# Kernel optimization log

Measured on AMD Instinct MI355X. Metric: run time of the kernel, lower is better.

Reference implementation:

```python
import jax, jax.numpy as jnp
import numpy as np

B, N, M = 2, 2048, 8192
C1, C = 256, 128
K, SHARE = 16, 8
BN_EPS = 1e-5


def bn(x, g, b):
    # eval-mode BatchNorm1d with running_mean=0, running_var=1
    return x * (g / jnp.sqrt(1.0 + BN_EPS)) + b


def setup_inputs() -> dict:
    key = jax.random.key(0)
    ks = iter(jax.random.split(key, 64))
    nrm = lambda shape, s=0.05: jax.random.normal(next(ks), shape, dtype=jnp.float32) * s
    ones = lambda n: jnp.ones((n,), jnp.float32)
    zeros = lambda n: jnp.zeros((n,), jnp.float32)
    CS = C // SHARE  # 16
    return {
        # forward args
        "xyz": jax.random.uniform(next(ks), (B, N, 3), dtype=jnp.float32),
        "feature": jax.random.normal(next(ks), (B, C1, N), dtype=jnp.float32),
        "target_xyz": jax.random.uniform(next(ks), (B, M, 3), dtype=jnp.float32),
        "target_feature": jax.random.normal(next(ks), (B, C, M), dtype=jnp.float32),
        # TransitionUp (is_head=False): two Conv1d(k=1, bias=False)+BN+ReLU
        "tu_lin1_w": nrm((C, C1)), "tu_bn1_g": ones(C), "tu_bn1_b": zeros(C),
        "tu_lin2_w": nrm((C, C)), "tu_bn2_g": ones(C), "tu_bn2_b": zeros(C),
        # PointTransformerBlock(128,128, share_planes=8, nsample=16)
        "blk_lin1_w": nrm((C, C)), "blk_bn1_g": ones(C), "blk_bn1_b": zeros(C),
        "wq": nrm((C, C)), "bq": zeros(C),
        "wk": nrm((C, C)), "bk": zeros(C),
        "wv": nrm((C, C)), "bv": zeros(C),
        # position MLP: Linear(3,3)+BN+ReLU+Linear(3,C)
        "p1_w": nrm((3, 3), 0.3), "p1_b": zeros(3), "p_bn_g": ones(3), "p_bn_b": zeros(3),
        "p2_w": nrm((C, 3), 0.3), "p2_b": zeros(C),
        # attention weight MLP: BN(C)+ReLU+Linear(C,CS)+BN(CS)+ReLU+Linear(CS,CS)
        "w_bn1_g": ones(C), "w_bn1_b": zeros(C),
        "w_lin1_w": nrm((CS, C)), "w_lin1_b": zeros(CS),
        "w_bn2_g": ones(CS), "w_bn2_b": zeros(CS),
        "w_lin2_w": nrm((CS, CS)), "w_lin2_b": zeros(CS),
        "blk_bn2_g": ones(C), "blk_bn2_b": zeros(C),
        "blk_lin3_w": nrm((C, C)), "blk_bn3_g": ones(C), "blk_bn3_b": zeros(C),
    }


def reference(xyz, feature, target_xyz, target_feature,
              tu_lin1_w, tu_bn1_g, tu_bn1_b, tu_lin2_w, tu_bn2_g, tu_bn2_b,
              blk_lin1_w, blk_bn1_g, blk_bn1_b,
              wq, bq, wk, bk, wv, bv,
              p1_w, p1_b, p_bn_g, p_bn_b, p2_w, p2_b,
              w_bn1_g, w_bn1_b, w_lin1_w, w_lin1_b, w_bn2_g, w_bn2_b, w_lin2_w, w_lin2_b,
              blk_bn2_g, blk_bn2_b, blk_lin3_w, blk_bn3_g, blk_bn3_b):
    # ---------------- TransitionUp (feature upsampling N -> M) ----------------
    # three_nn: 3 nearest source points for each target point
    d2 = jnp.sum((target_xyz[:, :, None, :] - xyz[:, None, :, :]) ** 2, -1)  # [B,M,N]
    negd, idx3 = jax.lax.top_k(-d2, 3)                                       # [B,M,3]
    dist = jnp.sqrt(jnp.maximum(-negd, 0.0))
    rec = 1.0 / (dist + 1e-8)
    weight = rec / jnp.sum(rec, -1, keepdims=True)                           # [B,M,3]

    f = jnp.einsum('oc,bcn->bon', tu_lin1_w, feature)                        # [B,C,N]
    f = jax.nn.relu(bn(f, tu_bn1_g[None, :, None], tu_bn1_b[None, :, None]))

    # three_interpolate: weighted gather of 3-NN features
    gath = jax.vmap(lambda fb, ib: fb[:, ib])(f, idx3)                       # [B,C,M,3]
    interp = jnp.sum(gath * weight[:, None, :, :], -1)                       # [B,C,M]

    tf = jnp.einsum('oc,bcm->bom', tu_lin2_w, target_feature)
    tf = jax.nn.relu(bn(tf, tu_bn2_g[None, :, None], tu_bn2_b[None, :, None]))
    feat = tf + interp                                                        # [B,C,M]

    # ---------------- PointTransformerBlock (local kNN vector attention) ----------------
    x = feat.transpose(0, 2, 1)                                               # [B,M,C]
    identity = x
    x1 = jax.nn.relu(bn(x @ blk_lin1_w.T, blk_bn1_g, blk_bn1_b))              # [B,M,C]

    # kNN among target points (includes self, distance 0)
    d2t = jnp.sum((target_xyz[:, :, None, :] - target_xyz[:, None, :, :]) ** 2, -1)  # [B,M,M]
    _, knn = jax.lax.top_k(-d2t, K)                                           # [B,M,K]

    q = x1 @ wq.T + bq
    k = x1 @ wk.T + bk
    v = x1 @ wv.T + bv
    gather_nb = jax.vmap(lambda tb, ib: tb[ib])                               # [M,C],[M,K] -> [M,K,C]
    xk = gather_nb(k, knn)                                                    # [B,M,K,C]
    xv = gather_nb(v, knn)                                                    # [B,M,K,C]

    # relative positional encoding
    pr = gather_nb(target_xyz, knn) - target_xyz[:, :, None, :]               # [B,M,K,3]
    pr = jax.nn.relu(bn(pr @ p1_w.T + p1_b, p_bn_g, p_bn_b)) @ p2_w.T + p2_b  # [B,M,K,C]

    r = xk - q[:, :, None, :] + pr                                            # [B,M,K,C]
    w = jax.nn.relu(bn(r, w_bn1_g, w_bn1_b)) @ w_lin1_w.T + w_lin1_b          # [B,M,K,CS]
    w = jax.nn.relu(bn(w, w_bn2_g, w_bn2_b)) @ w_lin2_w.T + w_lin2_b          # [B,M,K,CS]
    w = jax.nn.softmax(w, axis=2)                                             # over K neighbors

    CS = C // SHARE
    agg = jnp.sum((xv + pr).reshape(B, M, K, SHARE, CS) * w[:, :, :, None, :], axis=2)
    agg = agg.reshape(B, M, C)

    x2 = jax.nn.relu(bn(agg, blk_bn2_g, blk_bn2_b))
    x3 = bn(x2 @ blk_lin3_w.T, blk_bn3_g, blk_bn3_b)
    out = jax.nn.relu(x3 + identity)                                          # [B,M,C]
    return out.transpose(0, 2, 1)                                             # [B,C,M]
```

## Files before the change

### kernel.cpp

```cpp
#include <hip/hip_runtime.h>
#include <cstddef>
#include <cstdint>

#define B_  2
#define N_  2048
#define M_  8192
#define C1_ 256
#define C_  128
#define K_  16
#define CS_ 16

#define BNINV 0.9999950000374997f

#define LDSA 17
#define LDSB 33

__device__ __forceinline__ void stage_direct64(float4* Ls4, const float4* src4,
                                               size_t row_stride4, int k0,
                                               size_t col0_4, int t)
{
#pragma unroll
    for (int i = 0; i < 2; ++i) {
        int idx = t + i * 256;
        int kk = idx >> 4, f4 = idx & 15;
        Ls4[kk * LDSA + f4] = src4[(size_t)(k0 + kk) * row_stride4 + col0_4 + f4];
    }
}

__device__ __forceinline__ void stage_transposeA(float* Lsf, const float* src,
                                                 int row0, int ldk, int k0, int t)
{
    int u = t & 7, r = t >> 3;
#pragma unroll
    for (int i = 0; i < 2; ++i) {
        int row = r + i * 32;
        float4 v = *(const float4*)(src + (size_t)(row0 + row) * ldk + k0 + u * 4);
        Lsf[(u * 4 + 0) * 68 + row] = v.x;
        Lsf[(u * 4 + 1) * 68 + row] = v.y;
        Lsf[(u * 4 + 2) * 68 + row] = v.z;
        Lsf[(u * 4 + 3) * 68 + row] = v.w;
    }
}

__device__ __forceinline__ void stage_transposeB(float* Lsf, const float* src,
                                                 int ldk, int k0, int t)
{
    int u = t & 7, r = t >> 3;
#pragma unroll
    for (int i = 0; i < 4; ++i) {
        int row = r + i * 32;
        float4 v = *(const float4*)(src + (size_t)row * ldk + k0 + u * 4);
        Lsf[(u * 4 + 0) * 132 + row] = v.x;
        Lsf[(u * 4 + 1) * 132 + row] = v.y;
        Lsf[(u * 4 + 2) * 132 + row] = v.z;
        Lsf[(u * 4 + 3) * 132 + row] = v.w;
    }
}

__device__ __forceinline__ void gemm_step64(const float4* As4, const float4* Bs4,
                                            int tm, int tn, float acc[4][8])
{
#pragma unroll 4
    for (int kk = 0; kk < 32; ++kk) {
        float4 a0 = As4[kk * LDSA + tm];
        float4 b0 = Bs4[kk * LDSB + tn * 2];
        float4 b1 = Bs4[kk * LDSB + tn * 2 + 1];
        float av[4] = {a0.x,a0.y,a0.z,a0.w};
        float bv[8] = {b0.x,b0.y,b0.z,b0.w,b1.x,b1.y,b1.z,b1.w};
#pragma unroll
        for (int i = 0; i < 4; ++i)
#pragma unroll
            for (int j = 0; j < 8; ++j)
                acc[i][j] = fmaf(av[i], bv[j], acc[i][j]);
    }
}

__device__ __forceinline__ void load8(const float* p, float* v)
{
    float4 a = *(const float4*)p, b = *(const float4*)(p + 4);
    v[0]=a.x; v[1]=a.y; v[2]=a.z; v[3]=a.w; v[4]=b.x; v[5]=b.y; v[6]=b.z; v[7]=b.w;
}
__device__ __forceinline__ void store8(float* p, const float* v)
{
    *(float4*)p       = make_float4(v[0],v[1],v[2],v[3]);
    *(float4*)(p + 4) = make_float4(v[4],v[5],v[6],v[7]);
}

extern "C" __global__ __launch_bounds__(256) void k_f(
    const float* __restrict__ feature, const float* __restrict__ w,
    const float* __restrict__ g, const float* __restrict__ bb,
    float* __restrict__ f_t)
{
    __shared__ float4 As4[32 * LDSA], Bs4[32 * LDSB];
    int t = threadIdx.x, tm = t >> 4, tn = t & 15;
    int m0 = blockIdx.x * 64;
    int b = m0 >> 11;
    size_t col0_4 = (size_t)(m0 & (N_ - 1)) >> 2;
    const float4* src4 = (const float4*)feature + (size_t)b * C1_ * (N_ / 4);
    float acc[4][8] = {};
    for (int k0 = 0; k0 < C1_; k0 += 32) {
        stage_direct64(As4, src4, N_ / 4, k0, col0_4, t);
        stage_transposeB((float*)Bs4, w, C1_, k0, t);
        __syncthreads();
        gemm_step64(As4, Bs4, tm, tn, acc);
        __syncthreads();
    }
    int c0 = tn * 8;
    float gc[8], bc[8];
    load8(g + c0, gc); load8(bb + c0, bc);
#pragma unroll
    for (int mm = 0; mm < 4; ++mm) {
        int m = m0 + tm * 4 + mm;
        float o[8];
#pragma unroll
        for (int j = 0; j < 8; ++j)
            o[j] = fmaxf(fmaf(acc[mm][j], gc[j] * BNINV, bc[j]), 0.f);
        store8(f_t + (size_t)m * C_ + c0, o);
    }
}

extern "C" __global__ __launch_bounds__(256) void k_soa(
    const float* __restrict__ txyz,
    float* __restrict__ cx, float* __restrict__ cy, float* __restrict__ cz)
{
    int t = blockIdx.x * 256 + threadIdx.x;
    if (t < B_ * M_) {
        cx[t] = txyz[t*3+0];
        cy[t] = txyz[t*3+1];
        cz[t] = txyz[t*3+2];
    }
}

extern "C" __global__ __launch_bounds__(256) void k_three_nn(
    const float* __restrict__ xyz, const float* __restrict__ txyz,
    int* __restrict__ idx3, float* __restrict__ w3)
{
    int q    = blockIdx.x * 4 + (threadIdx.x >> 6);
    int lane = threadIdx.x & 63;
    int b    = q / M_;
    const float* src = xyz + (size_t)b * N_ * 3;
    float qx = txyz[(size_t)q*3+0], qy = txyz[(size_t)q*3+1], qz = txyz[(size_t)q*3+2];

    unsigned long long p0 = ~0ULL, p1 = ~0ULL, p2 = ~0ULL;
    for (int i = 0; i < N_/64; ++i) {
        int j = lane + (i << 6);
        float dx = src[j*3+0]-qx, dy = src[j*3+1]-qy, dz = src[j*3+2]-qz;
        float d = __fadd_rn(__fadd_rn(__fmul_rn(dx,dx), __fmul_rn(dy,dy)), __fmul_rn(dz,dz));
        unsigned long long key = ((unsigned long long)__float_as_uint(d) << 32) | (unsigned)j;
        if (key < p2) {
            p2 = key;
            if (p2 < p1) { unsigned long long t = p1; p1 = p2; p2 = t; }
            if (p1 < p0) { unsigned long long t = p0; p0 = p1; p1 = t; }
        }
    }
    unsigned long long wmin[3];
    unsigned long long h = p0;
#pragma unroll
    for (int r = 0; r < 3; ++r) {
        unsigned long long w = h;
#pragma unroll
        for (int s = 1; s < 64; s <<= 1) {
            unsigned long long o = __shfl_xor(w, s, 64);
            w = (o < w) ? o : w;
        }
        wmin[r] = w;
        if (h == w) { p0 = p1; p1 = p2; p2 = ~0ULL; h = p0; }
    }
    if (lane == 0) {
        float d0 = __uint_as_float((unsigned)(wmin[0] >> 32));
        float d1 = __uint_as_float((unsigned)(wmin[1] >> 32));
        float d2 = __uint_as_float((unsigned)(wmin[2] >> 32));
        float s0 = sqrtf(fmaxf(d0, 0.f)), s1 = sqrtf(fmaxf(d1, 0.f)), s2 = sqrtf(fmaxf(d2, 0.f));
        float r0 = 1.f/(s0+1e-8f), r1 = 1.f/(s1+1e-8f), r2 = 1.f/(s2+1e-8f);
        float inv = 1.f/(r0+r1+r2);
        idx3[(size_t)q*3+0] = (int)(unsigned)wmin[0];
        idx3[(size_t)q*3+1] = (int)(unsigned)wmin[1];
        idx3[(size_t)q*3+2] = (int)(unsigned)wmin[2];
        w3[(size_t)q*3+0] = r0*inv; w3[(size_t)q*3+1] = r1*inv; w3[(size_t)q*3+2] = r2*inv;
    }
}

extern "C" __global__ __launch_bounds__(256) void k_feat(
    const float* __restrict__ tfeat, const float* __restrict__ w2,
    const float* __restrict__ g, const float* __restrict__ bb,
    const float* __restrict__ f_t, const int* __restrict__ idx3,
    const float* __restrict__ w3, float* __restrict__ x)
{
    __shared__ float4 As4[32 * LDSA], Bs4[32 * LDSB];
    int t = threadIdx.x, tm = t >> 4, tn = t & 15;
    int m0 = blockIdx.x * 64;
    int b = m0 >> 13;
    size_t col0_4 = (size_t)(m0 & (M_ - 1)) >> 2;
    const float4* src4 = (const float4*)tfeat + (size_t)b * C_ * (M_ / 4);
    float acc[4][8] = {};
    for (int k0 = 0; k0 < C_; k0 += 32) {
        stage_direct64(As4, src4, M_ / 4, k0, col0_4, t);
        stage_transposeB((float*)Bs4, w2, C_, k0, t);
        __syncthreads();
        gemm_step64(As4, Bs4, tm, tn, acc);
        __syncthreads();
    }
    int c0 = tn * 8;
    float gc[8], bc[8];
    load8(g + c0, gc); load8(bb + c0, bc);
    const float* fb = f_t + (size_t)b * N_ * C_;
#pragma unroll
    for (int mm = 0; mm < 4; ++mm) {
        int m = m0 + tm * 4 + mm;
        int   i0 = idx3[m*3+0], i1 = idx3[m*3+1], i2 = idx3[m*3+2];
        float u0 = w3[m*3+0],  u1 = w3[m*3+1],  u2 = w3[m*3+2];
        float r0[8], r1[8], r2[8];
        load8(fb + (size_t)i0 * C_ + c0, r0);
        load8(fb + (size_t)i1 * C_ + c0, r1);
        load8(fb + (size_t)i2 * C_ + c0, r2);
        float o[8];
#pragma unroll
        for (int j = 0; j < 8; ++j) {
            float y = fmaxf(fmaf(acc[mm][j], gc[j] * BNINV, bc[j]), 0.f);
            o[j] = y + u0 * r0[j] + u1 * r1[j] + u2 * r2[j];
        }
        store8(x + (size_t)m * C_ + c0, o);
    }
}

extern "C" __global__ __launch_bounds__(256) void k_knn(
    const float* __restrict__ cx, const float* __restrict__ cy,
    const float* __restrict__ cz, int* __restrict__ out_knn)
{
    int q    = blockIdx.x * 4 + (threadIdx.x >> 6);
    int lane = threadIdx.x & 63;
    int b    = q >> 13;
    const float4* bx4 = (const float4*)(cx + (size_t)b * M_);
    const float4* by4 = (const float4*)(cy + (size_t)b * M_);
    const float4* bz4 = (const float4*)(cz + (size_t)b * M_);
    float qx = cx[q], qy = cy[q], qz = cz[q];

    unsigned long long list = ~0ULL;
    unsigned long long tau  = ~0ULL;
    float taud = 3e38f;

#define DIST(px,py,pz) ({ \
    float dx = (px)-qx, dy = (py)-qy, dz = (pz)-qz; \
    __fadd_rn(__fadd_rn(__fmul_rn(dx,dx), __fmul_rn(dy,dy)), __fmul_rn(dz,dz)); })

#define MIN4 (min(min(k0,k1),min(k2,k3)))

#define MERGELOOP { \
    unsigned long long mask = __ballot(mk < tau); \
    while (mask) { \
        int srcl = (int)__ffsll((long long)mask) - 1; \
        unsigned long long kk = __shfl(mk, srcl, 64); \
        unsigned long long below = __ballot(list < kk) & 0xFFFFull; \
        int pos = __popcll(below); \
        unsigned long long sh = __shfl_up(list, 1, 64); \
        if (lane == pos)                  list = kk; \
        else if (lane > pos && lane < K_) list = sh; \
        tau = __shfl(list, K_ - 1, 64); \
        if (lane == srcl) { \
            if      (k0 == mk) k0 = ~0ULL; \
            else if (k1 == mk) k1 = ~0ULL; \
            else if (k2 == mk) k2 = ~0ULL; \
            else               k3 = ~0ULL; \
            mk = MIN4; \
        } \
        mask = __ballot(mk < tau); \
    } \
    taud = __uint_as_float((unsigned)(tau >> 32)); }

    {
        float4 px = bx4[lane], py = by4[lane], pz = bz4[lane];
        float d0 = DIST(px.x,py.x,pz.x);
        float d1 = DIST(px.y,py.y,pz.y);
        float d2 = DIST(px.z,py.z,pz.z);
        float d3 = DIST(px.w,py.w,pz.w);
        unsigned long long j0 = (unsigned)(lane*4);
        unsigned long long k0 = ((unsigned long long)__float_as_uint(d0) << 32) | (j0+0);
        unsigned long long k1 = ((unsigned long long)__float_as_uint(d1) << 32) | (j0+1);
        unsigned long long k2 = ((unsigned long long)__float_as_uint(d2) << 32) | (j0+2);
        unsigned long long k3 = ((unsigned long long)__float_as_uint(d3) << 32) | (j0+3);
        unsigned long long key = k0;
#pragma unroll
        for (int k = 2; k <= 64; k <<= 1) {
#pragma unroll
            for (int j = k >> 1; j > 0; j >>= 1) {
                unsigned long long o = __shfl_xor(key, j, 64);
                bool up  = ((lane & k) == 0);
                bool low = ((lane & j) == 0);
                bool keepmin = (low == up);
                unsigned long long mn = (o < key) ? o : key;
                unsigned long long mx = (o < key) ? key : o;
                key = keepmin ? mn : mx;
            }
        }
        if (lane < K_) list = key;
        tau  = __shfl(list, K_ - 1, 64);
        taud = __uint_as_float((unsigned)(tau >> 32));
        k0 = ~0ULL;
        unsigned long long mk = MIN4;
        MERGELOOP
    }

    for (int i = 1; i < M_/256; ++i) {
        float4 px = bx4[i*64 + lane];
        float4 py = by4[i*64 + lane];
        float4 pz = bz4[i*64 + lane];
        float d0 = DIST(px.x,py.x,pz.x);
        float d1 = DIST(px.y,py.y,pz.y);
        float d2 = DIST(px.z,py.z,pz.z);
        float d3 = DIST(px.w,py.w,pz.w);
        bool any = (d0 <= taud) | (d1 <= taud) | (d2 <= taud) | (d3 <= taud);
        if (__ballot(any)) {
            unsigned long long j0 = (unsigned)(i*256 + lane*4);
            unsigned long long k0 = ((unsigned long long)__float_as_uint(d0) << 32) | (j0+0);
            unsigned long long k1 = ((unsigned long long)__float_as_uint(d1) << 32) | (j0+1);
            unsigned long long k2 = ((unsigned long long)__float_as_uint(d2) << 32) | (j0+2);
            unsigned long long k3 = ((unsigned long long)__float_as_uint(d3) << 32) | (j0+3);
            unsigned long long mk = MIN4;
            MERGELOOP
        }
    }
#undef MERGELOOP
#undef MIN4
#undef DIST
    if (lane < K_)
        out_knn[(size_t)q*K_ + lane] = (int)(unsigned)list;
}

extern "C" __global__ __launch_bounds__(256) void k_lqkv(
    const float* __restrict__ xin,
    const float* __restrict__ w1, const float* __restrict__ g1, const float* __restrict__ b1,
    const float* __restrict__ wq, const float* __restrict__ bq,
    const float* __restrict__ wk, const float* __restrict__ bk,
    const float* __restrict__ wv, const float* __restrict__ bv,
    float* __restrict__ q, float* __restrict__ k, float* __restrict__ v)
{
    __shared__ float  Asf[128 * 68];
    __shared__ float4 Bs4[32 * LDSB];
    int t = threadIdx.x, tm = t >> 4, tn = t & 15;
    int m0 = blockIdx.x * 64;
    int c0 = tn * 8;

    for (int k0 = 0; k0 < C_; k0 += 32)
        stage_transposeA(Asf + k0 * 68, xin, m0, C_, k0, t);

    float acc[4][8] = {};
    for (int k0 = 0; k0 < C_; k0 += 32) {
        stage_transposeB((float*)Bs4, w1, C_, k0, t);
        __syncthreads();
        gemm_step64((const float4*)Asf + k0 * 17, Bs4, tm, tn, acc);
        __syncthreads();
    }
    {
        float gc[8], bc[8];
        load8(g1 + c0, gc); load8(b1 + c0, bc);
#pragma unroll
        for (int mm = 0; mm < 4; ++mm) {
            int ml = tm * 4 + mm;
#pragma unroll
            for (int j = 0; j < 8; ++j)
                Asf[(c0 + j) * 68 + ml] = fmaxf(fmaf(acc[mm][j], gc[j] * BNINV, bc[j]), 0.f);
        }
    }
    __syncthreads();

#pragma unroll 1
    for (int which = 0; which < 3; ++which) {
        const float* W  = (which == 0) ? wq : (which == 1) ? wk : wv;
        const float* bi = (which == 0) ? bq : (which == 1) ? bk : bv;
        float*       out= (which == 0) ? q  : (which == 1) ? k  : v;
        float acc2[4][8] = {};
        for (int k0 = 0; k0 < C_; k0 += 32) {
            stage_transposeB((float*)Bs4, W, C_, k0, t);
            __syncthreads();
            gemm_step64((const float4*)Asf + k0 * 17, Bs4, tm, tn, acc2);
            __syncthreads();
        }
        float bc[8];
        load8(bi + c0, bc);
#pragma unroll
        for (int mm = 0; mm < 4; ++mm) {
            int m = m0 + tm * 4 + mm;
            float o[8];
#pragma unroll
            for (int j = 0; j < 8; ++j) o[j] = acc2[mm][j] + bc[j];
            store8(out + (size_t)m * C_ + c0, o);
        }
    }
}

extern "C" __global__ __launch_bounds__(128) void k_attn2(
    const float* __restrict__ q, const float* __restrict__ kf, const float* __restrict__ vf,
    const int* __restrict__ knn, const float* __restrict__ txyz,
    const float* __restrict__ p1w, const float* __restrict__ p1b,
    const float* __restrict__ pbg, const float* __restrict__ pbb,
    const float* __restrict__ p2w, const float* __restrict__ p2b,
    const float* __restrict__ wb1g, const float* __restrict__ wb1b,
    const float* __restrict__ wl1, const float* __restrict__ wl1b,
    const float* __restrict__ wb2g, const float* __restrict__ wb2b,
    const float* __restrict__ wl2, const float* __restrict__ wl2b,
    const float* __restrict__ bn2g, const float* __restrict__ bn2b,
    float* __restrict__ x2out)
{
    __shared__ int   nbs[K_];
    __shared__ float scrd[K_][3];
    __shared__ float tshs[K_ * C_];
    __shared__ float svs [K_ * C_];
    __shared__ float wl1s[CS_ * 132];
    __shared__ float wl2s[CS_ * 17];
    __shared__ float ashs[K_ * 17];
    __shared__ float wshs[K_ * 17];

    int bm = blockIdx.x;
    int b  = bm >> 13;
    int c  = threadIdx.x;

#pragma unroll
    for (int i = 0; i < 16; ++i) {
        int idx = c + i * 128;
        wl1s[(idx >> 7) * 132 + (idx & 127)] = wl1[idx];
    }
    {
        int i1 = c, i2 = c + 128;
        if (i1 < 256) wl2s[(i1 >> 4) * 17 + (i1 & 15)] = wl2[i1];
        if (i2 < 256) wl2s[(i2 >> 4) * 17 + (i2 & 15)] = wl2[i2];
    }
    if (c < K_) nbs[c] = knn[(size_t)bm * K_ + c];
    __syncthreads();

    float kfv[K_], vfv[K_];
    const float* txb = txyz + (size_t)b * M_ * 3;
#pragma unroll
    for (int t = 0; t < K_; ++t) {
        size_t nrow = ((size_t)b * M_ + nbs[t]) * C_ + c;
        kfv[t] = kf[nrow];
        vfv[t] = vf[nrow];
    }
    if (c < 48) {
        int t = c / 3, comp = c - t * 3;
        scrd[t][comp] = txb[nbs[t] * 3 + comp];
    }

    float qc = q[(size_t)bm * C_ + c];
    float qx = txyz[(size_t)bm*3+0], qy = txyz[(size_t)bm*3+1], qz = txyz[(size_t)bm*3+2];
    float p2w0 = p2w[c*3+0], p2w1 = p2w[c*3+1], p2w2 = p2w[c*3+2], p2bc = p2b[c];
    float b1s = wb1g[c]*BNINV, b1b = wb1b[c];
    float a00=p1w[0],a01=p1w[1],a02=p1w[2],a10=p1w[3],a11=p1w[4],a12=p1w[5],a20=p1w[6],a21=p1w[7],a22=p1w[8];
    float pb0=p1b[0], pb1=p1b[1], pb2=p1b[2];
    float g0=pbg[0]*BNINV, g1=pbg[1]*BNINV, g2=pbg[2]*BNINV;
    float hb0=pbb[0], hb1=pbb[1], hb2=pbb[2];
    __syncthreads();

#pragma unroll
    for (int t = 0; t < K_; ++t) {
        float dx = scrd[t][0]-qx, dy = scrd[t][1]-qy, dz = scrd[t][2]-qz;
        float h0 = fmaxf(fmaf(fmaf(a02,dz, fmaf(a01,dy, fmaf(a00,dx, pb0))), g0, hb0), 0.f);
        float h1 = fmaxf(fmaf(fmaf(a12,dz, fmaf(a11,dy, fmaf(a10,dx, pb1))), g1, hb1), 0.f);
        float h2 = fmaxf(fmaf(fmaf(a22,dz, fmaf(a21,dy, fmaf(a20,dx, pb2))), g2, hb2), 0.f);
        float pr = fmaf(p2w2,h2, fmaf(p2w1,h1, fmaf(p2w0,h0, p2bc)));
        float r = kfv[t] - qc + pr;
        tshs[t*C_ + c] = fmaxf(fmaf(r, b1s, b1b), 0.f);
        svs [t*C_ + c] = vfv[t] + pr;
    }
    __syncthreads();

    {
        int s = c >> 3, u = c & 7;
        float w1b = wl1b[s], gg = wb2g[s]*BNINV, gb = wb2b[s];
        for (int nb = 0; nb < K_; ++nb) {
            float a = 0.f;
#pragma unroll
            for (int i = 0; i < 16; ++i)
                a = fmaf(wl1s[s*132 + u + 8*i], tshs[nb*C_ + u + 8*i], a);
            a += __shfl_down(a, 4, 8);
            a += __shfl_down(a, 2, 8);
            a += __shfl_down(a, 1, 8);
            if (u == 0)
                ashs[nb*17 + s] = fmaxf(fmaf(a + w1b, gg, gb), 0.f);
        }
    }
    __syncthreads();

    {
        int nb = c >> 3;
        int cs1 = c & 7, cs2 = (c & 7) + 8;
        float a1 = wl2b[cs1], a2 = wl2b[cs2];
#pragma unroll
        for (int j = 0; j < CS_; ++j) {
            float av = ashs[nb*17 + j];
            a1 = fmaf(wl2s[cs1*17 + j], av, a1);
            a2 = fmaf(wl2s[cs2*17 + j], av, a2);
        }
        wshs[nb*17 + cs1] = a1;
        wshs[nb*17 + cs2] = a2;
    }
    __syncthreads();

    if (c < CS_) {
        float mx = -3e38f;
#pragma unroll
        for (int nb = 0; nb < K_; ++nb) mx = fmaxf(mx, wshs[nb*17 + c]);
        float ssum = 0.f;
#pragma unroll
        for (int nb = 0; nb < K_; ++nb) {
            float e = __expf(wshs[nb*17 + c] - mx);
            wshs[nb*17 + c] = e; ssum += e;
        }
        float inv = 1.f / ssum;
#pragma unroll
        for (int nb = 0; nb < K_; ++nb) wshs[nb*17 + c] *= inv;
    }
    __syncthreads();

    float agg = 0.f;
    int cs = c & (CS_ - 1);
#pragma unroll
    for (int nb = 0; nb < K_; ++nb)
        agg = fmaf(svs[nb*C_ + c], wshs[nb*17 + cs], agg);
    float x2 = fmaxf(fmaf(agg, bn2g[c]*BNINV, bn2b[c]), 0.f);
    x2out[(size_t)bm * C_ + c] = x2;
}

extern "C" __global__ __launch_bounds__(256) void k_lin3(
    const float* __restrict__ x2, const float* __restrict__ w,
    const float* __restrict__ g, const float* __restrict__ bb,
    const float* __restrict__ xid, float* __restrict__ out)
{
    __shared__ float4 As4[32 * LDSA], Bs4[32 * LDSB];
    int t = threadIdx.x, tm = t >> 4, tn = t & 15;
    int m0 = blockIdx.x * 64;
    int b  = m0 >> 13;
    float acc[4][8] = {};
    for (int k0 = 0; k0 < C_; k0 += 32) {
        stage_transposeA((float*)As4, x2, m0, C_, k0, t);
        stage_transposeB((float*)Bs4, w, C_, k0, t);
        __syncthreads();
        gemm_step64(As4, Bs4, tm, tn, acc);
        __syncthreads();
    }
    int c0 = tn * 8;
    float gc[8], bc[8];
    load8(g + c0, gc); load8(bb + c0, bc);
#pragma unroll
    for (int mm = 0; mm < 4; ++mm) {
        int m = m0 + tm * 4 + mm;
        float idv[8];
        load8(xid + (size_t)m * C_ + c0, idv);
#pragma unroll
        for (int j = 0; j < 8; ++j) {
            float x3 = fmaf(acc[mm][j], gc[j] * BNINV, bc[j]);
            acc[mm][j] = fmaxf(x3 + idv[j], 0.f);
        }
    }
    int mloc = (m0 & (M_ - 1)) + tm * 4;
    float* ob = out + (size_t)b * C_ * M_;
#pragma unroll
    for (int j = 0; j < 8; ++j) {
        float* p = ob + (size_t)(c0 + j) * M_ + mloc;
        *(float4*)p = make_float4(acc[0][j], acc[1][j], acc[2][j], acc[3][j]);
    }
}

extern "C" void kernel_launch(void* const* d_in, const int* in_sizes, int n_in,
                              void* d_out, int out_size, void* d_ws, size_t ws_size,
                              hipStream_t stream)
{
    const float* xyz   = (const float*)d_in[0];
    const float* feat  = (const float*)d_in[1];
    const float* txyz  = (const float*)d_in[2];
    const float* tfeat = (const float*)d_in[3];
    const float* tu1w  = (const float*)d_in[4];
    const float* tu1g  = (const float*)d_in[5];
    const float* tu1b  = (const float*)d_in[6];
    const float* tu2w  = (const float*)d_in[7];
    const float* tu2g  = (const float*)d_in[8];
    const float* tu2b  = (const float*)d_in[9];
    const float* bl1w  = (const float*)d_in[10];
    const float* bl1g  = (const float*)d_in[11];
    const float* bl1b  = (const float*)d_in[12];
    const float* wq    = (const float*)d_in[13];
    const float* bq    = (const float*)d_in[14];
    const float* wk    = (const float*)d_in[15];
    const float* bk    = (const float*)d_in[16];
    const float* wv    = (const float*)d_in[17];
    const float* bv    = (const float*)d_in[18];
    const float* p1w   = (const float*)d_in[19];
    const float* p1b   = (const float*)d_in[20];
    const float* pbg   = (const float*)d_in[21];
    const float* pbb   = (const float*)d_in[22];
    const float* p2w   = (const float*)d_in[23];
    const float* p2b   = (const float*)d_in[24];
    const float* wb1g  = (const float*)d_in[25];
    const float* wb1b  = (const float*)d_in[26];
    const float* wl1   = (const float*)d_in[27];
    const float* wl1b  = (const float*)d_in[28];
    const float* wb2g  = (const float*)d_in[29];
    const float* wb2b  = (const float*)d_in[30];
    const float* wl2   = (const float*)d_in[31];
    const float* wl2b  = (const float*)d_in[32];
    const float* bn2g  = (const float*)d_in[33];
    const float* bn2b  = (const float*)d_in[34];
    const float* l3w   = (const float*)d_in[35];
    const float* bn3g  = (const float*)d_in[36];
    const float* bn3b  = (const float*)d_in[37];

    char* ws = (char*)d_ws;
    size_t off = 0;
    auto alloc = [&](size_t bytes) { void* p = ws + off; off += (bytes + 255) & ~(size_t)255; return p; };
    float* f_t  = (float*)alloc(sizeof(float) * B_ * N_ * C_);
    int*   idx3 = (int*)  alloc(sizeof(int)   * B_ * M_ * 3);
    float* w3   = (float*)alloc(sizeof(float) * B_ * M_ * 3);
    float* x    = (float*)alloc(sizeof(float) * B_ * M_ * C_);
    float* x2   = (float*)alloc(sizeof(float) * B_ * M_ * C_);
    float* qb   = (float*)alloc(sizeof(float) * B_ * M_ * C_);
    float* kb   = (float*)alloc(sizeof(float) * B_ * M_ * C_);
    float* vb   = (float*)alloc(sizeof(float) * B_ * M_ * C_);
    int*   knn  = (int*)  alloc(sizeof(int)   * B_ * M_ * K_);
    float* cx   = (float*)alloc(sizeof(float) * B_ * M_);
    float* cy   = (float*)alloc(sizeof(float) * B_ * M_);
    float* cz   = (float*)alloc(sizeof(float) * B_ * M_);

    k_soa     <<<(B_*M_+255)/256, 256, 0, stream>>>(txyz, cx, cy, cz);
    k_f       <<<B_*N_/64,        256, 0, stream>>>(feat, tu1w, tu1g, tu1b, f_t);
    k_three_nn<<<B_*M_/4,         256, 0, stream>>>(xyz, txyz, idx3, w3);
    k_feat    <<<B_*M_/64,        256, 0, stream>>>(tfeat, tu2w, tu2g, tu2b, f_t, idx3, w3, x);
    k_knn     <<<B_*M_/4,         256, 0, stream>>>(cx, cy, cz, knn);
    k_lqkv    <<<B_*M_/64,        256, 0, stream>>>(x, bl1w, bl1g, bl1b,
                                                    wq, bq, wk, bk, wv, bv, qb, kb, vb);
    k_attn2   <<<B_*M_,           128, 0, stream>>>(qb, kb, vb, knn, txyz,
                                                    p1w, p1b, pbg, pbb, p2w, p2b,
                                                    wb1g, wb1b, wl1, wl1b, wb2g, wb2b, wl2, wl2b,
                                                    bn2g, bn2b, x2);
    k_lin3    <<<B_*M_/64,        256, 0, stream>>>(x2, l3w, bn3g, bn3b, x, (float*)d_out);
}
```

Measured before the change: 374.0 us.

## Fuse independent kernels into heterogeneous launches splitting kNN across stages

The self-kNN search is split into three block ranges and co-scheduled inside three combined kernels, alongside the feature GEMM plus three-NN, the interpolation GEMM, and the QKV projection. Block index selects which body runs, so independent work fills the GPU concurrently instead of running serially. This removes launch gaps and tail underutilisation. The cost is a uniform register and LDS footprint across both roles, which may reduce occupancy for the lighter kNN blocks.

```diff
diff --git a/kernel.cpp b/kernel.cpp
--- a/kernel.cpp
+++ b/kernel.cpp
@@ -12,6 +12,14 @@
 
 #define BNINV 0.9999950000374997f
 
+#define KNN1 1024
+#define KNN2 2048
+#define KNN3 1024
+#define FB    (B_*N_/64)
+#define TNNB  (B_*M_/4)
+#define FEATB (B_*M_/64)
+#define LQKVB (B_*M_/64)
+
 #define LDSA 17
 #define LDSB 33
 
@@ -86,149 +94,13 @@
     *(float4*)(p + 4) = make_float4(v[4],v[5],v[6],v[7]);
 }
 
-extern "C" __global__ __launch_bounds__(256) void k_f(
-    const float* __restrict__ feature, const float* __restrict__ w,
-    const float* __restrict__ g, const float* __restrict__ bb,
-    float* __restrict__ f_t)
-{
-    __shared__ float4 As4[32 * LDSA], Bs4[32 * LDSB];
-    int t = threadIdx.x, tm = t >> 4, tn = t & 15;
-    int m0 = blockIdx.x * 64;
-    int b = m0 >> 11;
-    size_t col0_4 = (size_t)(m0 & (N_ - 1)) >> 2;
-    const float4* src4 = (const float4*)feature + (size_t)b * C1_ * (N_ / 4);
-    float acc[4][8] = {};
-    for (int k0 = 0; k0 < C1_; k0 += 32) {
-        stage_direct64(As4, src4, N_ / 4, k0, col0_4, t);
-        stage_transposeB((float*)Bs4, w, C1_, k0, t);
-        __syncthreads();
-        gemm_step64(As4, Bs4, tm, tn, acc);
-        __syncthreads();
-    }
-    int c0 = tn * 8;
-    float gc[8], bc[8];
-    load8(g + c0, gc); load8(bb + c0, bc);
-#pragma unroll
-    for (int mm = 0; mm < 4; ++mm) {
-        int m = m0 + tm * 4 + mm;
-        float o[8];
-#pragma unroll
-        for (int j = 0; j < 8; ++j)
-            o[j] = fmaxf(fmaf(acc[mm][j], gc[j] * BNINV, bc[j]), 0.f);
-        store8(f_t + (size_t)m * C_ + c0, o);
-    }
-}
-
-extern "C" __global__ __launch_bounds__(256) void k_soa(
-    const float* __restrict__ txyz,
-    float* __restrict__ cx, float* __restrict__ cy, float* __restrict__ cz)
-{
-    int t = blockIdx.x * 256 + threadIdx.x;
-    if (t < B_ * M_) {
-        cx[t] = txyz[t*3+0];
-        cy[t] = txyz[t*3+1];
-        cz[t] = txyz[t*3+2];
-    }
-}
-
-extern "C" __global__ __launch_bounds__(256) void k_three_nn(
-    const float* __restrict__ xyz, const float* __restrict__ txyz,
-    int* __restrict__ idx3, float* __restrict__ w3)
-{
-    int q    = blockIdx.x * 4 + (threadIdx.x >> 6);
-    int lane = threadIdx.x & 63;
-    int b    = q / M_;
-    const float* src = xyz + (size_t)b * N_ * 3;
-    float qx = txyz[(size_t)q*3+0], qy = txyz[(size_t)q*3+1], qz = txyz[(size_t)q*3+2];
-
-    unsigned long long p0 = ~0ULL, p1 = ~0ULL, p2 = ~0ULL;
-    for (int i = 0; i < N_/64; ++i) {
-        int j = lane + (i << 6);
-        float dx = src[j*3+0]-qx, dy = src[j*3+1]-qy, dz = src[j*3+2]-qz;
-        float d = __fadd_rn(__fadd_rn(__fmul_rn(dx,dx), __fmul_rn(dy,dy)), __fmul_rn(dz,dz));
-        unsigned long long key = ((unsigned long long)__float_as_uint(d) << 32) | (unsigned)j;
-        if (key < p2) {
-            p2 = key;
-            if (p2 < p1) { unsigned long long t = p1; p1 = p2; p2 = t; }
-            if (p1 < p0) { unsigned long long t = p0; p0 = p1; p1 = t; }
-        }
-    }
-    unsigned long long wmin[3];
-    unsigned long long h = p0;
-#pragma unroll
-    for (int r = 0; r < 3; ++r) {
-        unsigned long long w = h;
-#pragma unroll
-        for (int s = 1; s < 64; s <<= 1) {
-            unsigned long long o = __shfl_xor(w, s, 64);
-            w = (o < w) ? o : w;
-        }
-        wmin[r] = w;
-        if (h == w) { p0 = p1; p1 = p2; p2 = ~0ULL; h = p0; }
-    }
-    if (lane == 0) {
-        float d0 = __uint_as_float((unsigned)(wmin[0] >> 32));
-        float d1 = __uint_as_float((unsigned)(wmin[1] >> 32));
-        float d2 = __uint_as_float((unsigned)(wmin[2] >> 32));
-        float s0 = sqrtf(fmaxf(d0, 0.f)), s1 = sqrtf(fmaxf(d1, 0.f)), s2 = sqrtf(fmaxf(d2, 0.f));
-        float r0 = 1.f/(s0+1e-8f), r1 = 1.f/(s1+1e-8f), r2 = 1.f/(s2+1e-8f);
-        float inv = 1.f/(r0+r1+r2);
-        idx3[(size_t)q*3+0] = (int)(unsigned)wmin[0];
-        idx3[(size_t)q*3+1] = (int)(unsigned)wmin[1];
-        idx3[(size_t)q*3+2] = (int)(unsigned)wmin[2];
-        w3[(size_t)q*3+0] = r0*inv; w3[(size_t)q*3+1] = r1*inv; w3[(size_t)q*3+2] = r2*inv;
-    }
-}
-
-extern "C" __global__ __launch_bounds__(256) void k_feat(
-    const float* __restrict__ tfeat, const float* __restrict__ w2,
-    const float* __restrict__ g, const float* __restrict__ bb,
-    const float* __restrict__ f_t, const int* __restrict__ idx3,
-    const float* __restrict__ w3, float* __restrict__ x)
-{
-    __shared__ float4 As4[32 * LDSA], Bs4[32 * LDSB];
-    int t = threadIdx.x, tm = t >> 4, tn = t & 15;
-    int m0 = blockIdx.x * 64;
-    int b = m0 >> 13;
-    size_t col0_4 = (size_t)(m0 & (M_ - 1)) >> 2;
-    const float4* src4 = (const float4*)tfeat + (size_t)b * C_ * (M_ / 4);
-    float acc[4][8] = {};
-    for (int k0 = 0; k0 < C_; k0 += 32) {
-        stage_direct64(As4, src4, M_ / 4, k0, col0_4, t);
-        stage_transposeB((float*)Bs4, w2, C_, k0, t);
-        __syncthreads();
-        gemm_step64(As4, Bs4, tm, tn, acc);
-        __syncthreads();
-    }
-    int c0 = tn * 8;
-    float gc[8], bc[8];
-    load8(g + c0, gc); load8(bb + c0, bc);
-    const float* fb = f_t + (size_t)b * N_ * C_;
-#pragma unroll
-    for (int mm = 0; mm < 4; ++mm) {
-        int m = m0 + tm * 4 + mm;
-        int   i0 = idx3[m*3+0], i1 = idx3[m*3+1], i2 = idx3[m*3+2];
-        float u0 = w3[m*3+0],  u1 = w3[m*3+1],  u2 = w3[m*3+2];
-        float r0[8], r1[8], r2[8];
-        load8(fb + (size_t)i0 * C_ + c0, r0);
-        load8(fb + (size_t)i1 * C_ + c0, r1);
-        load8(fb + (size_t)i2 * C_ + c0, r2);
-        float o[8];
-#pragma unroll
-        for (int j = 0; j < 8; ++j) {
-            float y = fmaxf(fmaf(acc[mm][j], gc[j] * BNINV, bc[j]), 0.f);
-            o[j] = y + u0 * r0[j] + u1 * r1[j] + u2 * r2[j];
-        }
-        store8(x + (size_t)m * C_ + c0, o);
-    }
-}
-
-extern "C" __global__ __launch_bounds__(256) void k_knn(
-    const float* __restrict__ cx, const float* __restrict__ cy,
-    const float* __restrict__ cz, int* __restrict__ out_knn)
-{
-    int q    = blockIdx.x * 4 + (threadIdx.x >> 6);
-    int lane = threadIdx.x & 63;
+
+__device__ void knn_body(const float* __restrict__ cx, const float* __restrict__ cy,
+                         const float* __restrict__ cz, int* __restrict__ out_knn,
+                         int qblock, int tid)
+{
+    int q    = qblock * 4 + (tid >> 6);
+    int lane = tid & 63;
     int b    = q >> 13;
     const float4* bx4 = (const float4*)(cx + (size_t)b * M_);
     const float4* by4 = (const float4*)(cy + (size_t)b * M_);
@@ -326,18 +198,140 @@
         out_knn[(size_t)q*K_ + lane] = (int)(unsigned)list;
 }
 
-extern "C" __global__ __launch_bounds__(256) void k_lqkv(
-    const float* __restrict__ xin,
-    const float* __restrict__ w1, const float* __restrict__ g1, const float* __restrict__ b1,
-    const float* __restrict__ wq, const float* __restrict__ bq,
-    const float* __restrict__ wk, const float* __restrict__ bk,
-    const float* __restrict__ wv, const float* __restrict__ bv,
-    float* __restrict__ q, float* __restrict__ k, float* __restrict__ v)
-{
-    __shared__ float  Asf[128 * 68];
-    __shared__ float4 Bs4[32 * LDSB];
-    int t = threadIdx.x, tm = t >> 4, tn = t & 15;
-    int m0 = blockIdx.x * 64;
+__device__ void f_body(const float* __restrict__ feature, const float* __restrict__ w,
+                       const float* __restrict__ g, const float* __restrict__ bb,
+                       float* __restrict__ f_t, int m0, int t, char* smem)
+{
+    float4* As4 = (float4*)smem;
+    float4* Bs4 = (float4*)(smem + 32 * LDSA * 16);
+    int tm = t >> 4, tn = t & 15;
+    int b = m0 >> 11;
+    size_t col0_4 = (size_t)(m0 & (N_ - 1)) >> 2;
+    const float4* src4 = (const float4*)feature + (size_t)b * C1_ * (N_ / 4);
+    float acc[4][8] = {};
+    for (int k0 = 0; k0 < C1_; k0 += 32) {
+        stage_direct64(As4, src4, N_ / 4, k0, col0_4, t);
+        stage_transposeB((float*)Bs4, w, C1_, k0, t);
+        __syncthreads();
+        gemm_step64(As4, Bs4, tm, tn, acc);
+        __syncthreads();
+    }
+    int c0 = tn * 8;
+    float gc[8], bc[8];
+    load8(g + c0, gc); load8(bb + c0, bc);
+#pragma unroll
+    for (int mm = 0; mm < 4; ++mm) {
+        int m = m0 + tm * 4 + mm;
+        float o[8];
+#pragma unroll
+        for (int j = 0; j < 8; ++j)
+            o[j] = fmaxf(fmaf(acc[mm][j], gc[j] * BNINV, bc[j]), 0.f);
+        store8(f_t + (size_t)m * C_ + c0, o);
+    }
+}
+
+__device__ void tnn_body(const float* __restrict__ xyz, const float* __restrict__ txyz,
+                         int* __restrict__ idx3, float* __restrict__ w3,
+                         int q, int lane)
+{
+    int b = q / M_;
+    const float* src = xyz + (size_t)b * N_ * 3;
+    float qx = txyz[(size_t)q*3+0], qy = txyz[(size_t)q*3+1], qz = txyz[(size_t)q*3+2];
+
+    unsigned long long p0 = ~0ULL, p1 = ~0ULL, p2 = ~0ULL;
+    for (int i = 0; i < N_/64; ++i) {
+        int j = lane + (i << 6);
+        float dx = src[j*3+0]-qx, dy = src[j*3+1]-qy, dz = src[j*3+2]-qz;
+        float d = __fadd_rn(__fadd_rn(__fmul_rn(dx,dx), __fmul_rn(dy,dy)), __fmul_rn(dz,dz));
+        unsigned long long key = ((unsigned long long)__float_as_uint(d) << 32) | (unsigned)j;
+        if (key < p2) {
+            p2 = key;
+            if (p2 < p1) { unsigned long long t = p1; p1 = p2; p2 = t; }
+            if (p1 < p0) { unsigned long long t = p0; p0 = p1; p1 = t; }
+        }
+    }
+    unsigned long long wmin[3];
+    unsigned long long h = p0;
+#pragma unroll
+    for (int r = 0; r < 3; ++r) {
+        unsigned long long w = h;
+#pragma unroll
+        for (int s = 1; s < 64; s <<= 1) {
+            unsigned long long o = __shfl_xor(w, s, 64);
+            w = (o < w) ? o : w;
+        }
+        wmin[r] = w;
+        if (h == w) { p0 = p1; p1 = p2; p2 = ~0ULL; h = p0; }
+    }
+    if (lane == 0) {
+        float d0 = __uint_as_float((unsigned)(wmin[0] >> 32));
+        float d1 = __uint_as_float((unsigned)(wmin[1] >> 32));
+        float d2 = __uint_as_float((unsigned)(wmin[2] >> 32));
+        float s0 = sqrtf(fmaxf(d0, 0.f)), s1 = sqrtf(fmaxf(d1, 0.f)), s2 = sqrtf(fmaxf(d2, 0.f));
+        float r0 = 1.f/(s0+1e-8f), r1 = 1.f/(s1+1e-8f), r2 = 1.f/(s2+1e-8f);
+        float inv = 1.f/(r0+r1+r2);
+        idx3[(size_t)q*3+0] = (int)(unsigned)wmin[0];
+        idx3[(size_t)q*3+1] = (int)(unsigned)wmin[1];
+        idx3[(size_t)q*3+2] = (int)(unsigned)wmin[2];
+        w3[(size_t)q*3+0] = r0*inv; w3[(size_t)q*3+1] = r1*inv; w3[(size_t)q*3+2] = r2*inv;
+    }
+}
+
+__device__ void feat_body(const float* __restrict__ tfeat, const float* __restrict__ w2,
+                          const float* __restrict__ g, const float* __restrict__ bb,
+                          const float* __restrict__ f_t, const int* __restrict__ idx3,
+                          const float* __restrict__ w3, float* __restrict__ x,
+                          int m0, int t, char* smem)
+{
+    float4* As4 = (float4*)smem;
+    float4* Bs4 = (float4*)(smem + 32 * LDSA * 16);
+    int tm = t >> 4, tn = t & 15;
+    int b = m0 >> 13;
+    size_t col0_4 = (size_t)(m0 & (M_ - 1)) >> 2;
+    const float4* src4 = (const float4*)tfeat + (size_t)b * C_ * (M_ / 4);
+    float acc[4][8] = {};
+    for (int k0 = 0; k0 < C_; k0 += 32) {
+        stage_direct64(As4, src4, M_ / 4, k0, col0_4, t);
+        stage_transposeB((float*)Bs4, w2, C_, k0, t);
+        __syncthreads();
+        gemm_step64(As4, Bs4, tm, tn, acc);
+        __syncthreads();
+    }
+    int c0 = tn * 8;
+    float gc[8], bc[8];
+    load8(g + c0, gc); load8(bb + c0, bc);
+    const float* fb = f_t + (size_t)b * N_ * C_;
+#pragma unroll
+    for (int mm = 0; mm < 4; ++mm) {
+        int m = m0 + tm * 4 + mm;
+        int   i0 = idx3[m*3+0], i1 = idx3[m*3+1], i2 = idx3[m*3+2];
+        float u0 = w3[m*3+0],  u1 = w3[m*3+1],  u2 = w3[m*3+2];
+        float r0[8], r1[8], r2[8];
+        load8(fb + (size_t)i0 * C_ + c0, r0);
+        load8(fb + (size_t)i1 * C_ + c0, r1);
+        load8(fb + (size_t)i2 * C_ + c0, r2);
+        float o[8];
+#pragma unroll
+        for (int j = 0; j < 8; ++j) {
+            float y = fmaxf(fmaf(acc[mm][j], gc[j] * BNINV, bc[j]), 0.f);
+            o[j] = y + u0 * r0[j] + u1 * r1[j] + u2 * r2[j];
+        }
+        store8(x + (size_t)m * C_ + c0, o);
+    }
+}
+
+__device__ void lqkv_body(const float* __restrict__ xin,
+                          const float* __restrict__ w1, const float* __restrict__ g1,
+                          const float* __restrict__ b1,
+                          const float* __restrict__ wq, const float* __restrict__ bq,
+                          const float* __restrict__ wk, const float* __restrict__ bk,
+                          const float* __restrict__ wv, const float* __restrict__ bv,
+                          float* __restrict__ q, float* __restrict__ k, float* __restrict__ v,
+                          int m0, int t, char* smem)
+{
+    float*  Asf = (float*)smem;
+    float4* Bs4 = (float4*)(smem + 128 * 68 * 4);
+    int tm = t >> 4, tn = t & 15;
     int c0 = tn * 8;
 
     for (int k0 = 0; k0 < C_; k0 += 32)
@@ -386,6 +380,73 @@
             store8(out + (size_t)m * C_ + c0, o);
         }
     }
+}
+
+
+extern "C" __global__ __launch_bounds__(256) void k_soa(
+    const float* __restrict__ txyz,
+    float* __restrict__ cx, float* __restrict__ cy, float* __restrict__ cz)
+{
+    int t = blockIdx.x * 256 + threadIdx.x;
+    if (t < B_ * M_) {
+        cx[t] = txyz[t*3+0];
+        cy[t] = txyz[t*3+1];
+        cz[t] = txyz[t*3+2];
+    }
+}
+
+extern "C" __global__ __launch_bounds__(256) void k_fat1(
+    const float* __restrict__ cx, const float* __restrict__ cy,
+    const float* __restrict__ cz, int* __restrict__ out_knn,
+    const float* __restrict__ feature, const float* __restrict__ w,
+    const float* __restrict__ g, const float* __restrict__ bb,
+    float* __restrict__ f_t,
+    const float* __restrict__ xyz, const float* __restrict__ txyz,
+    int* __restrict__ idx3, float* __restrict__ w3)
+{
+    __shared__ __align__(16) char smem[32 * LDSA * 16 + 32 * LDSB * 16];
+    int bid = blockIdx.x, tid = threadIdx.x;
+    if (bid < KNN1)
+        knn_body(cx, cy, cz, out_knn, bid, tid);
+    else if (bid < KNN1 + FB)
+        f_body(feature, w, g, bb, f_t, (bid - KNN1) * 64, tid, smem);
+    else
+        tnn_body(xyz, txyz, idx3, w3, (bid - KNN1 - FB) * 4 + (tid >> 6), tid & 63);
+}
+
+extern "C" __global__ __launch_bounds__(256) void k_fat2(
+    const float* __restrict__ cx, const float* __restrict__ cy,
+    const float* __restrict__ cz, int* __restrict__ out_knn,
+    const float* __restrict__ tfeat, const float* __restrict__ w2,
+    const float* __restrict__ g, const float* __restrict__ bb,
+    const float* __restrict__ f_t, const int* __restrict__ idx3,
+    const float* __restrict__ w3, float* __restrict__ x)
+{
+    __shared__ __align__(16) char smem[32 * LDSA * 16 + 32 * LDSB * 16];
+    int bid = blockIdx.x, tid = threadIdx.x;
+    if (bid < KNN2)
+        knn_body(cx, cy, cz, out_knn, KNN1 + bid, tid);
+    else
+        feat_body(tfeat, w2, g, bb, f_t, idx3, w3, x, (bid - KNN2) * 64, tid, smem);
+}
+
+extern "C" __global__ __launch_bounds__(256) void k_fat3(
+    const float* __restrict__ cx, const float* __restrict__ cy,
+    const float* __restrict__ cz, int* __restrict__ out_knn,
+    const float* __restrict__ xin,
+    const float* __restrict__ w1, const float* __restrict__ g1, const float* __restrict__ b1,
+    const float* __restrict__ wq, const float* __restrict__ bq,
+    const float* __restrict__ wk, const float* __restrict__ bk,
+    const float* __restrict__ wv, const float* __restrict__ bv,
+    float* __restrict__ q, float* __restrict__ k, float* __restrict__ v)
+{
+    __shared__ __align__(16) char smem[128 * 68 * 4 + 32 * LDSB * 16];
+    int bid = blockIdx.x, tid = threadIdx.x;
+    if (bid < KNN3)
+        knn_body(cx, cy, cz, out_knn, KNN1 + KNN2 + bid, tid);
+    else
+        lqkv_body(xin, w1, g1, b1, wq, bq, wk, bk, wv, bv, q, k, v,
+                  (bid - KNN3) * 64, tid, smem);
 }
 
 extern "C" __global__ __launch_bounds__(128) void k_attn2(
@@ -619,16 +680,19 @@
     float* cy   = (float*)alloc(sizeof(float) * B_ * M_);
     float* cz   = (float*)alloc(sizeof(float) * B_ * M_);
 
-    k_soa     <<<(B_*M_+255)/256, 256, 0, stream>>>(txyz, cx, cy, cz);
-    k_f       <<<B_*N_/64,        256, 0, stream>>>(feat, tu1w, tu1g, tu1b, f_t);
-    k_three_nn<<<B_*M_/4,         256, 0, stream>>>(xyz, txyz, idx3, w3);
-    k_feat    <<<B_*M_/64,        256, 0, stream>>>(tfeat, tu2w, tu2g, tu2b, f_t, idx3, w3, x);
-    k_knn     <<<B_*M_/4,         256, 0, stream>>>(cx, cy, cz, knn);
-    k_lqkv    <<<B_*M_/64,        256, 0, stream>>>(x, bl1w, bl1g, bl1b,
-                                                    wq, bq, wk, bk, wv, bv, qb, kb, vb);
-    k_attn2   <<<B_*M_,           128, 0, stream>>>(qb, kb, vb, knn, txyz,
-                                                    p1w, p1b, pbg, pbb, p2w, p2b,
-                                                    wb1g, wb1b, wl1, wl1b, wb2g, wb2b, wl2, wl2b,
-                                                    bn2g, bn2b, x2);
-    k_lin3    <<<B_*M_/64,        256, 0, stream>>>(x2, l3w, bn3g, bn3b, x, (float*)d_out);
-}
+    k_soa  <<<(B_*M_+255)/256,     256, 0, stream>>>(txyz, cx, cy, cz);
+    k_fat1 <<<KNN1 + FB + TNNB,    256, 0, stream>>>(cx, cy, cz, knn,
+                                                     feat, tu1w, tu1g, tu1b, f_t,
+                                                     xyz, txyz, idx3, w3);
+    k_fat2 <<<KNN2 + FEATB,        256, 0, stream>>>(cx, cy, cz, knn,
+                                                     tfeat, tu2w, tu2g, tu2b,
+                                                     f_t, idx3, w3, x);
+    k_fat3 <<<KNN3 + LQKVB,        256, 0, stream>>>(cx, cy, cz, knn,
+                                                     x, bl1w, bl1g, bl1b,
+                                                     wq, bq, wk, bk, wv, bv, qb, kb, vb);
+    k_attn2<<<B_*M_,               128, 0, stream>>>(qb, kb, vb, knn, txyz,
+                                                     p1w, p1b, pbg, pbb, p2w, p2b,
+                                                     wb1g, wb1b, wl1, wl1b, wb2g, wb2b, wl2, wl2b,
+                                                     bn2g, bn2b, x2);
+    k_lin3 <<<B_*M_/64,            256, 0, stream>>>(x2, l3w, bn3g, bn3b, x, (float*)d_out);
+}
```

Result: slower. 427.7 us (+14.4%).

## Process two query points per attention block and keep value rows in registers

Applied to the files above, without the earlier changes.

The attention kernel now handles two target points per 256-thread block instead of one per 128-thread block. This halves the number of times the shared wl1/wl2 weight tiles are loaded into LDS per point. The value-plus-positional term is also kept in registers instead of a shared svs array, which removes that LDS traffic and its footprint. In exchange the per-block LDS for tshs/ashs/wshs doubles and register pressure rises slightly, which may change occupancy.

```diff
diff --git a/kernel.cpp b/kernel.cpp
--- a/kernel.cpp
+++ b/kernel.cpp
@@ -388,7 +388,7 @@
     }
 }
 
-extern "C" __global__ __launch_bounds__(128) void k_attn2(
+extern "C" __global__ __launch_bounds__(256) void k_attn2(
     const float* __restrict__ q, const float* __restrict__ kf, const float* __restrict__ vf,
     const int* __restrict__ knn, const float* __restrict__ txyz,
     const float* __restrict__ p1w, const float* __restrict__ p1b,
@@ -401,43 +401,40 @@
     const float* __restrict__ bn2g, const float* __restrict__ bn2b,
     float* __restrict__ x2out)
 {
-    __shared__ int   nbs[K_];
-    __shared__ float scrd[K_][3];
-    __shared__ float tshs[K_ * C_];
-    __shared__ float svs [K_ * C_];
+    __shared__ int   nbs[2][K_];
+    __shared__ float scrd[2][K_][3];
+    __shared__ float tshs[2][K_ * C_];
     __shared__ float wl1s[CS_ * 132];
     __shared__ float wl2s[CS_ * 17];
-    __shared__ float ashs[K_ * 17];
-    __shared__ float wshs[K_ * 17];
-
-    int bm = blockIdx.x;
-    int b  = bm >> 13;
-    int c  = threadIdx.x;
-
-#pragma unroll
-    for (int i = 0; i < 16; ++i) {
-        int idx = c + i * 128;
+    __shared__ float ashs[2][K_ * 17];
+    __shared__ float wshs[2][K_ * 17];
+
+    int tid = threadIdx.x;
+    int p   = tid >> 7;
+    int c   = tid & 127;
+    int bm  = blockIdx.x * 2 + p;
+    int b   = bm >> 13;
+
+#pragma unroll
+    for (int i = 0; i < 8; ++i) {
+        int idx = tid + i * 256;
         wl1s[(idx >> 7) * 132 + (idx & 127)] = wl1[idx];
     }
-    {
-        int i1 = c, i2 = c + 128;
-        if (i1 < 256) wl2s[(i1 >> 4) * 17 + (i1 & 15)] = wl2[i1];
-        if (i2 < 256) wl2s[(i2 >> 4) * 17 + (i2 & 15)] = wl2[i2];
-    }
-    if (c < K_) nbs[c] = knn[(size_t)bm * K_ + c];
+    wl2s[(tid >> 4) * 17 + (tid & 15)] = wl2[tid & 255];
+    if (c < K_) nbs[p][c] = knn[(size_t)bm * K_ + c];
     __syncthreads();
 
-    float kfv[K_], vfv[K_];
+    float kfv[K_], svr[K_];
     const float* txb = txyz + (size_t)b * M_ * 3;
 #pragma unroll
     for (int t = 0; t < K_; ++t) {
-        size_t nrow = ((size_t)b * M_ + nbs[t]) * C_ + c;
+        size_t nrow = ((size_t)b * M_ + nbs[p][t]) * C_ + c;
         kfv[t] = kf[nrow];
-        vfv[t] = vf[nrow];
+        svr[t] = vf[nrow];
     }
     if (c < 48) {
         int t = c / 3, comp = c - t * 3;
-        scrd[t][comp] = txb[nbs[t] * 3 + comp];
+        scrd[p][t][comp] = txb[nbs[p][t] * 3 + comp];
     }
 
     float qc = q[(size_t)bm * C_ + c];
@@ -452,14 +449,14 @@
 
 #pragma unroll
     for (int t = 0; t < K_; ++t) {
-        float dx = scrd[t][0]-qx, dy = scrd[t][1]-qy, dz = scrd[t][2]-qz;
+        float dx = scrd[p][t][0]-qx, dy = scrd[p][t][1]-qy, dz = scrd[p][t][2]-qz;
         float h0 = fmaxf(fmaf(fmaf(a02,dz, fmaf(a01,dy, fmaf(a00,dx, pb0))), g0, hb0), 0.f);
         float h1 = fmaxf(fmaf(fmaf(a12,dz, fmaf(a11,dy, fmaf(a10,dx, pb1))), g1, hb1), 0.f);
         float h2 = fmaxf(fmaf(fmaf(a22,dz, fmaf(a21,dy, fmaf(a20,dx, pb2))), g2, hb2), 0.f);
         float pr = fmaf(p2w2,h2, fmaf(p2w1,h1, fmaf(p2w0,h0, p2bc)));
         float r = kfv[t] - qc + pr;
-        tshs[t*C_ + c] = fmaxf(fmaf(r, b1s, b1b), 0.f);
-        svs [t*C_ + c] = vfv[t] + pr;
+        tshs[p][t*C_ + c] = fmaxf(fmaf(r, b1s, b1b), 0.f);
+        svr[t] += pr;
     }
     __syncthreads();
 
@@ -470,12 +467,12 @@
             float a = 0.f;
 #pragma unroll
             for (int i = 0; i < 16; ++i)
-                a = fmaf(wl1s[s*132 + u + 8*i], tshs[nb*C_ + u + 8*i], a);
+                a = fmaf(wl1s[s*132 + u + 8*i], tshs[p][nb*C_ + u + 8*i], a);
             a += __shfl_down(a, 4, 8);
             a += __shfl_down(a, 2, 8);
             a += __shfl_down(a, 1, 8);
             if (u == 0)
-                ashs[nb*17 + s] = fmaxf(fmaf(a + w1b, gg, gb), 0.f);
+                ashs[p][nb*17 + s] = fmaxf(fmaf(a + w1b, gg, gb), 0.f);
         }
     }
     __syncthreads();
@@ -486,28 +483,28 @@
         float a1 = wl2b[cs1], a2 = wl2b[cs2];
 #pragma unroll
         for (int j = 0; j < CS_; ++j) {
-            float av = ashs[nb*17 + j];
+            float av = ashs[p][nb*17 + j];
             a1 = fmaf(wl2s[cs1*17 + j], av, a1);
             a2 = fmaf(wl2s[cs2*17 + j], av, a2);
         }
-        wshs[nb*17 + cs1] = a1;
-        wshs[nb*17 + cs2] = a2;
+        wshs[p][nb*17 + cs1] = a1;
+        wshs[p][nb*17 + cs2] = a2;
     }
     __syncthreads();
 
     if (c < CS_) {
         float mx = -3e38f;
 #pragma unroll
-        for (int nb = 0; nb < K_; ++nb) mx = fmaxf(mx, wshs[nb*17 + c]);
+        for (int nb = 0; nb < K_; ++nb) mx = fmaxf(mx, wshs[p][nb*17 + c]);
         float ssum = 0.f;
 #pragma unroll
         for (int nb = 0; nb < K_; ++nb) {
-            float e = __expf(wshs[nb*17 + c] - mx);
-            wshs[nb*17 + c] = e; ssum += e;
+            float e = __expf(wshs[p][nb*17 + c] - mx);
+            wshs[p][nb*17 + c] = e; ssum += e;
         }
         float inv = 1.f / ssum;
 #pragma unroll
-        for (int nb = 0; nb < K_; ++nb) wshs[nb*17 + c] *= inv;
+        for (int nb = 0; nb < K_; ++nb) wshs[p][nb*17 + c] *= inv;
     }
     __syncthreads();
 
@@ -515,7 +512,7 @@
     int cs = c & (CS_ - 1);
 #pragma unroll
     for (int nb = 0; nb < K_; ++nb)
-        agg = fmaf(svs[nb*C_ + c], wshs[nb*17 + cs], agg);
+        agg = fmaf(svr[nb], wshs[p][nb*17 + cs], agg);
     float x2 = fmaxf(fmaf(agg, bn2g[c]*BNINV, bn2b[c]), 0.f);
     x2out[(size_t)bm * C_ + c] = x2;
 }
@@ -626,7 +623,7 @@
     k_knn     <<<B_*M_/4,         256, 0, stream>>>(cx, cy, cz, knn);
     k_lqkv    <<<B_*M_/64,        256, 0, stream>>>(x, bl1w, bl1g, bl1b,
                                                     wq, bq, wk, bk, wv, bv, qb, kb, vb);
-    k_attn2   <<<B_*M_,           128, 0, stream>>>(qb, kb, vb, knn, txyz,
+    k_attn2   <<<B_*M_/2,         256, 0, stream>>>(qb, kb, vb, knn, txyz,
                                                     p1w, p1b, pbg, pbb, p2w, p2b,
                                                     wb1g, wb1b, wl1, wl1b, wb2g, wb2b, wl2, wl2b,
                                                     bn2g, bn2b, x2);
```

Result: faster. 339.7 us (median of 2 runs) (-9.2%).
